# Kernel tuning notes

Measured on AMD Instinct MI355X. Metric: run time of the kernel, lower is better.

Reference implementation:

```python
import jax, jax.numpy as jnp
import numpy as np

B, K = 512, 64
EBD, VFD = 256, 512
SENS = EBD + VFD            # 768 sensory inputs to layer 0
LAYERS = [512, 256, 64]     # inter, command, motor neurons (NCP wiring)


def _make_layer_params(key, in_features, hidden):
    ks = jax.random.split(key, 9)
    cat = in_features + hidden
    s = 1.0 / np.sqrt(cat)
    def lin(k):
        return jax.random.normal(k, (hidden, cat), dtype=jnp.float32) * s
    # sparsity mask: random NCP-style sparsity on the input block, dense recurrent block
    in_mask = (jax.random.uniform(ks[8], (hidden, in_features)) < 0.5).astype(jnp.float32)
    rec_mask = jnp.ones((hidden, hidden), dtype=jnp.float32)
    mask = jnp.concatenate([in_mask, rec_mask], axis=1)  # (hidden, in+hidden)
    return dict(
        ff1_w=lin(ks[0]), ff1_b=jnp.zeros((hidden,), jnp.float32),
        ff2_w=lin(ks[1]), ff2_b=jnp.zeros((hidden,), jnp.float32),
        ta_w=lin(ks[2]), ta_b=jnp.zeros((hidden,), jnp.float32),
        tb_w=lin(ks[3]), tb_b=jnp.zeros((hidden,), jnp.float32),
        mask=mask,
    )


def setup_inputs() -> dict:
    key = jax.random.key(0)
    k_base, k_vis, k0, k1, k2 = jax.random.split(key, 5)
    inp = {
        'base_expanded_seq': jax.random.normal(k_base, (B, K, EBD), dtype=jnp.float32),
        'visual_seq': jax.random.normal(k_vis, (B, K, VFD), dtype=jnp.float32),
    }
    in_feats = [SENS, LAYERS[0], LAYERS[1]]
    for li, (k, fin, hid) in enumerate(zip([k0, k1, k2], in_feats, LAYERS)):
        p = _make_layer_params(k, fin, hid)
        for name, v in p.items():
            inp[f'l{li}_{name}'] = v
    return inp


def _cfc_cell(x_in, h, ff1_w, ff1_b, ff2_w, ff2_b, ta_w, ta_b, tb_w, tb_b, mask, ts=1.0):
    # ncps CfCCell, mode='default', no backbone, sparsity mask on ff1/ff2
    x = jnp.concatenate([x_in, h], axis=-1)          # (B, in+hidden)
    ff1 = jnp.tanh(x @ (ff1_w * mask).T + ff1_b)
    ff2 = jnp.tanh(x @ (ff2_w * mask).T + ff2_b)
    t_a = x @ ta_w.T + ta_b
    t_b = x @ tb_w.T + tb_b
    t_interp = jax.nn.sigmoid(t_a * ts + t_b)
    return ff1 * (1.0 - t_interp) + t_interp * ff2


def reference(base_expanded_seq, visual_seq,
              l0_ff1_w, l0_ff1_b, l0_ff2_w, l0_ff2_b, l0_ta_w, l0_ta_b, l0_tb_w, l0_tb_b, l0_mask,
              l1_ff1_w, l1_ff1_b, l1_ff2_w, l1_ff2_b, l1_ta_w, l1_ta_b, l1_tb_w, l1_tb_b, l1_mask,
              l2_ff1_w, l2_ff1_b, l2_ff2_w, l2_ff2_b, l2_ta_w, l2_ta_b, l2_tb_w, l2_tb_b, l2_mask):
    layers = [
        (l0_ff1_w, l0_ff1_b, l0_ff2_w, l0_ff2_b, l0_ta_w, l0_ta_b, l0_tb_w, l0_tb_b, l0_mask),
        (l1_ff1_w, l1_ff1_b, l1_ff2_w, l1_ff2_b, l1_ta_w, l1_ta_b, l1_tb_w, l1_tb_b, l1_mask),
        (l2_ff1_w, l2_ff1_b, l2_ff2_w, l2_ff2_b, l2_ta_w, l2_ta_b, l2_tb_w, l2_tb_b, l2_mask),
    ]
    b = base_expanded_seq.shape[0]
    x_seq = jnp.concatenate([base_expanded_seq, visual_seq], axis=-1)  # (B,K,768)
    x_seq = jnp.swapaxes(x_seq, 0, 1)                                  # (K,B,768)
    h_init = tuple(jnp.zeros((b, h), dtype=x_seq.dtype) for h in LAYERS)

    def step(carry, x_t):
        inp = x_t
        new_hs = []
        for p, h in zip(layers, carry):
            h_new = _cfc_cell(inp, h, *p)
            inp = h_new
            new_hs.append(h_new)
        return tuple(new_hs), None

    final_h, _ = jax.lax.scan(step, h_init, x_seq)
    return final_h[-1]  # (B, motor_neurons) = last timestep motor-layer output
```

## Files before the change

### kernel.cpp

```cpp
#include <hip/hip_runtime.h>
#include <cmath>


typedef __attribute__((ext_vector_type(8))) _Float16 half8;
typedef __attribute__((ext_vector_type(4))) float f32x4;

#define DEVINL __device__ __forceinline__

struct Params {
  const float* base;
  const float* visual;
  const _Float16 *w0, *w1, *w2;
  const float *b0f1,*b0f2,*b0ta,*b0tb;
  const float *b1f1,*b1f2,*b1ta,*b1tb;
  const float *b2f1,*b2f2,*b2ta,*b2tb;
  _Float16 *xh0,*xl0,*xh1,*xl1;
  float *xacc0,*xacc1;
  _Float16 *h0h0,*h0h1,*h0l0,*h0l1;
  _Float16 *h1h0,*h1h1,*h1l0,*h1l1;
  _Float16 *h2h0,*h2h1,*h2l0,*h2l1;
  float* out;
};

DEVINL void gload(half8& d, const _Float16* a) {
  asm volatile("global_load_dwordx4 %0, %1, off" : "=v"(d) : "v"(a));
}
template <int V>
DEVINL void vmwait() {
  __builtin_amdgcn_s_waitcnt((V & 15) | (7 << 4) | (15 << 8) | ((V >> 4) << 14));
  __builtin_amdgcn_sched_barrier(0);
}

template <int C, int NC, int D, class AF>
DEVINL void pipe_iter(half8 (&buf)[D][6], f32x4 (&acc)[4], const AF& addr) {
  constexpr int issued = (C + D < NC) ? (C + D) : NC;
  vmwait<6 * (issued - C - 1)>();
  {
    half8 b0 = buf[C % D][0], b1 = buf[C % D][1];
    half8 b2 = buf[C % D][2], b3 = buf[C % D][3];
    half8 ah = buf[C % D][4], al = buf[C % D][5];
    acc[0] = __builtin_amdgcn_mfma_f32_16x16x32_f16(ah, b0, acc[0], 0, 0, 0);
    acc[0] = __builtin_amdgcn_mfma_f32_16x16x32_f16(al, b0, acc[0], 0, 0, 0);
    acc[1] = __builtin_amdgcn_mfma_f32_16x16x32_f16(ah, b1, acc[1], 0, 0, 0);
    acc[1] = __builtin_amdgcn_mfma_f32_16x16x32_f16(al, b1, acc[1], 0, 0, 0);
    acc[2] = __builtin_amdgcn_mfma_f32_16x16x32_f16(ah, b2, acc[2], 0, 0, 0);
    acc[2] = __builtin_amdgcn_mfma_f32_16x16x32_f16(al, b2, acc[2], 0, 0, 0);
    acc[3] = __builtin_amdgcn_mfma_f32_16x16x32_f16(ah, b3, acc[3], 0, 0, 0);
    acc[3] = __builtin_amdgcn_mfma_f32_16x16x32_f16(al, b3, acc[3], 0, 0, 0);
  }
  if constexpr (C + D < NC) {
#pragma unroll
    for (int j = 0; j < 6; ++j) gload(buf[C % D][j], addr(C + D, j));
  }
  if constexpr (C + 1 < NC) pipe_iter<C + 1, NC, D>(buf, acc, addr);
}

template <int NC, class AF>
DEVINL void gemm_pipe(f32x4 (&acc)[4], const AF& addr) {
  constexpr int D = (NC < 6) ? NC : 6;
  half8 buf[D][6];
#pragma unroll
  for (int c = 0; c < D; ++c)
#pragma unroll
    for (int j = 0; j < 6; ++j) gload(buf[c][j], addr(c, j));
  pipe_iter<0, NC, D>(buf, acc, addr);
}

DEVINL void run_xprep(const Params& p, int t, int b ) {
  _Float16* xh = (t & 1) ? p.xh1 : p.xh0;
  _Float16* xl = (t & 1) ? p.xl1 : p.xl0;
  int tid = b * 256 + threadIdx.x;
#pragma unroll
  for (int i = tid; i < 49152; i += 12288) {
    int m = i / 96;
    int k = (i - m * 96) * 8;
    const float* src = (k < 256) ? (p.base + (m * 64 + t) * 256 + k)
                                 : (p.visual + (m * 64 + t) * 512 + (k - 256));
    const f32x4* q = (const f32x4*)src;
    f32x4 v0 = q[0], v1 = q[1];
    half8 hh, ll;
#pragma unroll
    for (int j = 0; j < 4; ++j) {
      _Float16 a = (_Float16)v0[j]; hh[j] = a;     ll[j]     = (_Float16)(v0[j] - (float)a);
      _Float16 c = (_Float16)v1[j]; hh[j + 4] = c; ll[j + 4] = (_Float16)(v1[j] - (float)c);
    }
    int off = (((m >> 4) * 24 + (k >> 5)) * 64 + ((k >> 3) & 3) * 16 + (m & 15)) * 8;
    *(half8*)(xh + off) = hh;
    *(half8*)(xl + off) = ll;
  }
}

DEVINL void run_xgemm(const Params& p, int t, int b ) {
  const _Float16* xh = (t & 1) ? p.xh1 : p.xh0;
  const _Float16* xl = (t & 1) ? p.xl1 : p.xl0;
  float* xacc = (t & 1) ? p.xacc1 : p.xacc0;
  const int lane = threadIdx.x & 63, wv = threadIdx.x >> 6;
  const int lr = lane & 15, lq = lane >> 4;
  const int mt = b >> 5, nt = b & 31;
  const int m_base = mt * 64 + wv * 16, n0 = nt * 16;
  const int mt16 = mt * 4 + wv;

  f32x4 acc[4];
#pragma unroll
  for (int g = 0; g < 4; ++g) acc[g] = f32x4{0.f, 0.f, 0.f, 0.f};

  const _Float16* wpk = p.w0 + (nt * 40) * 512 + lane * 8;
  const _Float16* apk = xh + (mt16 * 24) * 512 + lane * 8;
  const _Float16* lpk = xl + (mt16 * 24) * 512 + lane * 8;
  auto addr = [&](int c, int j) -> const _Float16* {
    if (j < 4) return wpk + (j * (32 * 40) + c) * 512;
    return ((j == 4) ? apk : lpk) + c * 512;
  };
  gemm_pipe<24>(acc, addr);

  const int n = n0 + lr;
  const int mrow = m_base + lq * 4;
#pragma unroll
  for (int g = 0; g < 4; ++g)
#pragma unroll
    for (int r = 0; r < 4; ++r)
      xacc[(mrow + r) * 2048 + g * 512 + n] = acc[g][r];
}

template <int L>
DEVINL void run_rec(const Params& p, int t, int b) {
  constexpr int HH = (L == 0) ? 512 : ((L == 1) ? 256 : 64);
  constexpr int NC = (L == 0) ? 16 : ((L == 1) ? 24 : 10);
  constexpr int NCH = HH / 32;

  const int lane = threadIdx.x & 63, wv = threadIdx.x >> 6;
  const int lr = lane & 15, lq = lane >> 4;
  int mt, nt;
  if constexpr (L == 0)      { mt = b >> 5; nt = b & 31; }
  else if constexpr (L == 1) { mt = b >> 4; nt = b & 15; }
  else                       { mt = b >> 2; nt = b & 3; }
  const int m_base = mt * 64 + wv * 16, n0 = nt * 16;
  const int mt16 = mt * 4 + wv;
  const int wbuf = t & 1;

  const _Float16 *hph, *hpl, *pah = nullptr, *pal = nullptr;
  _Float16 *oh, *ol;
  const float *bf1p, *bf2p, *btap, *btbp;
  const _Float16* wpk;
  if constexpr (L == 0) {
    wpk = p.w0 + (nt * 40) * 512 + lane * 8;
    hph = wbuf ? p.h0h0 : p.h0h1;  hpl = wbuf ? p.h0l0 : p.h0l1;
    oh  = wbuf ? p.h0h1 : p.h0h0;  ol  = wbuf ? p.h0l1 : p.h0l0;
    bf1p = p.b0f1; bf2p = p.b0f2; btap = p.b0ta; btbp = p.b0tb;
  } else if constexpr (L == 1) {
    wpk = p.w1 + (nt * 24) * 512 + lane * 8;
    pah = wbuf ? p.h0h1 : p.h0h0;  pal = wbuf ? p.h0l1 : p.h0l0;
    hph = wbuf ? p.h1h0 : p.h1h1;  hpl = wbuf ? p.h1l0 : p.h1l1;
    oh  = wbuf ? p.h1h1 : p.h1h0;  ol  = wbuf ? p.h1l1 : p.h1l0;
    bf1p = p.b1f1; bf2p = p.b1f2; btap = p.b1ta; btbp = p.b1tb;
  } else {
    wpk = p.w2 + (nt * 10) * 512 + lane * 8;
    pah = wbuf ? p.h1h1 : p.h1h0;  pal = wbuf ? p.h1l1 : p.h1l0;
    hph = wbuf ? p.h2h0 : p.h2h1;  hpl = wbuf ? p.h2l0 : p.h2l1;
    oh  = wbuf ? p.h2h1 : p.h2h0;  ol  = wbuf ? p.h2l1 : p.h2l0;
    bf1p = p.b2f1; bf2p = p.b2f2; btap = p.b2ta; btbp = p.b2tb;
  }

  f32x4 acc[4];
#pragma unroll
  for (int g = 0; g < 4; ++g) acc[g] = f32x4{0.f, 0.f, 0.f, 0.f};

  const int lane8 = lane * 8;
  auto addr = [&](int c, int j) -> const _Float16* {
    if constexpr (L == 0) {
      if (j < 4) return wpk + (j * (32 * 40) + 24 + c) * 512;
      return ((j == 4) ? hph : hpl) + (mt16 * 16 + c) * 512 + lane8;
    } else if constexpr (L == 1) {
      if (j < 4) return wpk + (j * (16 * 24) + c) * 512;
      if (c < 16) return ((j == 4) ? pah : pal) + (mt16 * 16 + c) * 512 + lane8;
      return ((j == 4) ? hph : hpl) + (mt16 * 8 + (c - 16)) * 512 + lane8;
    } else {
      if (j < 4) return wpk + (j * (4 * 10) + c) * 512;
      if (c < 8) return ((j == 4) ? pah : pal) + (mt16 * 8 + c) * 512 + lane8;
      return ((j == 4) ? hph : hpl) + (mt16 * 2 + (c - 8)) * 512 + lane8;
    }
  };
  gemm_pipe<NC>(acc, addr);

  const float* xacc = nullptr;
  if constexpr (L == 0) xacc = (t & 1) ? p.xacc1 : p.xacc0;

  const int n = n0 + lr;
  const float bff1 = bf1p[n], bff2 = bf2p[n], bta = btap[n], btb = btbp[n];
  const int obase = ((m_base >> 4) * NCH + (n >> 5)) * 512 + ((n >> 3) & 3) * 128 + (n & 7);
#pragma unroll
  for (int r = 0; r < 4; ++r) {
    const int row = m_base + lq * 4 + r;
    const int lrr = lq * 4 + r;
    float a0 = acc[0][r], a1 = acc[1][r], a2 = acc[2][r], a3 = acc[3][r];
    if constexpr (L == 0) {
      const float* xb = xacc + row * 2048 + n;
      a0 += xb[0]; a1 += xb[512]; a2 += xb[1024]; a3 += xb[1536];
    }
    float vf1 = a0 + bff1;
    float vf2 = a1 + bff2;
    float vt  = (a2 + bta) + (a3 + btb);
    float ff1 = tanhf(vf1);
    float ff2 = tanhf(vf2);
    float ti  = 1.0f / (1.0f + __expf(-vt));
    float hv  = ff1 + ti * (ff2 - ff1);
    _Float16 hh = (_Float16)hv;
    oh[obase + lrr * 8] = hh;
    ol[obase + lrr * 8] = (_Float16)(hv - (float)hh);
    if constexpr (L == 2) {
      if (t == 63) p.out[row * 64 + n] = hv;
    }
  }
}

__global__ __launch_bounds__(256, 2) void cfc_step(Params p, int s) {
  const int bid = blockIdx.x;
  if (bid < 48)       { int t = s + 2; if (t >= 0 && t < 64) run_xprep(p, t, bid); }
  else if (bid < 304) { int t = s + 1; if (t >= 0 && t < 64) run_xgemm(p, t, bid - 48); }
  else if (bid < 560) { int t = s;     if (t >= 0 && t < 64) run_rec<0>(p, t, bid - 304); }
  else if (bid < 688) { int t = s - 1; if (t >= 0 && t < 64) run_rec<1>(p, t, bid - 560); }
  else                { int t = s - 2; if (t >= 0 && t < 64) run_rec<2>(p, t, bid - 688); }
}

__global__ void prep_w_pk(const float* __restrict__ w, const float* __restrict__ mask,
                          _Float16* __restrict__ dst, int WK, int total) {
  int i = blockIdx.x * 256 + threadIdx.x;
  if (i >= total) return;
  int e = i & 7, lane = (i >> 3) & 63, rem = i >> 9;
  int NCk = WK >> 5;
  int c = rem % NCk, nt = rem / NCk;
  int n = nt * 16 + (lane & 15);
  int k = c * 32 + (lane >> 4) * 8 + e;
  float v = w[n * WK + k];
  if (mask) v *= mask[n * WK + k];
  dst[i] = (_Float16)v;
}

__global__ void zero_kernel(unsigned* __restrict__ p, int n) {
  int i = blockIdx.x * 256 + threadIdx.x;
  if (i < n) p[i] = 0u;
}

extern "C" void kernel_launch(void* const* d_in, const int* in_sizes, int n_in,
                              void* d_out, int out_size, void* d_ws, size_t ws_size,
                              hipStream_t stream) {
  _Float16* w0  = (_Float16*)d_ws;
  _Float16* w1  = w0 + 2621440;
  _Float16* w2  = w1 + 786432;
  _Float16* xh0 = w2 + 81920;
  _Float16* xl0 = xh0 + 393216;
  _Float16* xh1 = xl0 + 393216;
  _Float16* xl1 = xh1 + 393216;
  _Float16* hb  = xl1 + 393216;
  _Float16* h0h0 = hb;            _Float16* h0h1 = h0h0 + 262144;
  _Float16* h0l0 = h0h1 + 262144; _Float16* h0l1 = h0l0 + 262144;
  _Float16* h1h0 = h0l1 + 262144; _Float16* h1h1 = h1h0 + 131072;
  _Float16* h1l0 = h1h1 + 131072; _Float16* h1l1 = h1l0 + 131072;
  _Float16* h2h0 = h1l1 + 131072; _Float16* h2h1 = h2h0 + 32768;
  _Float16* h2l0 = h2h1 + 32768;  _Float16* h2l1 = h2l0 + 32768;
  float* xacc0 = (float*)(h2l1 + 32768);
  float* xacc1 = xacc0 + 1048576;

  const int h_uints = 1703936 / 2;
  zero_kernel<<<(h_uints + 255) / 256, 256, 0, stream>>>((unsigned*)hb, h_uints);

  const float* F = nullptr;
  auto in = [&](int i) { return (const float*)d_in[i]; };

  prep_w_pk<<<2560, 256, 0, stream>>>(in(2),  in(10), w0 + 0 * 655360, 1280, 655360);
  prep_w_pk<<<2560, 256, 0, stream>>>(in(4),  in(10), w0 + 1 * 655360, 1280, 655360);
  prep_w_pk<<<2560, 256, 0, stream>>>(in(6),  F,      w0 + 2 * 655360, 1280, 655360);
  prep_w_pk<<<2560, 256, 0, stream>>>(in(8),  F,      w0 + 3 * 655360, 1280, 655360);
  prep_w_pk<<<768,  256, 0, stream>>>(in(11), in(19), w1 + 0 * 196608, 768,  196608);
  prep_w_pk<<<768,  256, 0, stream>>>(in(13), in(19), w1 + 1 * 196608, 768,  196608);
  prep_w_pk<<<768,  256, 0, stream>>>(in(15), F,      w1 + 2 * 196608, 768,  196608);
  prep_w_pk<<<768,  256, 0, stream>>>(in(17), F,      w1 + 3 * 196608, 768,  196608);
  prep_w_pk<<<80,   256, 0, stream>>>(in(20), in(28), w2 + 0 * 20480,  320,  20480);
  prep_w_pk<<<80,   256, 0, stream>>>(in(22), in(28), w2 + 1 * 20480,  320,  20480);
  prep_w_pk<<<80,   256, 0, stream>>>(in(24), F,      w2 + 2 * 20480,  320,  20480);
  prep_w_pk<<<80,   256, 0, stream>>>(in(26), F,      w2 + 3 * 20480,  320,  20480);

  Params p;
  p.base = in(0); p.visual = in(1);
  p.w0 = w0; p.w1 = w1; p.w2 = w2;
  p.b0f1 = in(3);  p.b0f2 = in(5);  p.b0ta = in(7);  p.b0tb = in(9);
  p.b1f1 = in(12); p.b1f2 = in(14); p.b1ta = in(16); p.b1tb = in(18);
  p.b2f1 = in(21); p.b2f2 = in(23); p.b2ta = in(25); p.b2tb = in(27);
  p.xh0 = xh0; p.xl0 = xl0; p.xh1 = xh1; p.xl1 = xl1;
  p.xacc0 = xacc0; p.xacc1 = xacc1;
  p.h0h0 = h0h0; p.h0h1 = h0h1; p.h0l0 = h0l0; p.h0l1 = h0l1;
  p.h1h0 = h1h0; p.h1h1 = h1h1; p.h1l0 = h1l0; p.h1l1 = h1l1;
  p.h2h0 = h2h0; p.h2h1 = h2h1; p.h2l0 = h2l0; p.h2l1 = h2l1;
  p.out = (float*)d_out;

  for (int s = -2; s < 66; ++s) {
    cfc_step<<<720, 256, 0, stream>>>(p, s);
  }
}
```

Baseline: 1.216 ms.

## Widen per-wave GEMM tile to 64 rows to reuse weight fragments

Each wave now computes four 16-row sub-tiles against the same four weight fragments, so weight loads are reused across 64 batch rows instead of 16. The grid shrinks from 720 to 216 blocks and the load pipeline depth drops from 6 to 2 stages of 12 loads each. This cuts redundant weight traffic, but it raises register pressure (64 accumulator floats plus 24 buffered half8s) and leaves fewer blocks to hide latency across the CUs.

Result: slower. 1.361 ms (+12.0%).

```diff
diff --git a/kernel.cpp b/kernel.cpp
--- a/kernel.cpp
+++ b/kernel.cpp
@@ -32,37 +32,37 @@
 }
 
 template <int C, int NC, int D, class AF>
-DEVINL void pipe_iter(half8 (&buf)[D][6], f32x4 (&acc)[4], const AF& addr) {
+DEVINL void pipe_iter(half8 (&buf)[D][12], f32x4 (&acc)[4][4], const AF& addr) {
   constexpr int issued = (C + D < NC) ? (C + D) : NC;
-  vmwait<6 * (issued - C - 1)>();
+  vmwait<12 * (issued - C - 1)>();
   {
-    half8 b0 = buf[C % D][0], b1 = buf[C % D][1];
-    half8 b2 = buf[C % D][2], b3 = buf[C % D][3];
-    half8 ah = buf[C % D][4], al = buf[C % D][5];
-    acc[0] = __builtin_amdgcn_mfma_f32_16x16x32_f16(ah, b0, acc[0], 0, 0, 0);
-    acc[0] = __builtin_amdgcn_mfma_f32_16x16x32_f16(al, b0, acc[0], 0, 0, 0);
-    acc[1] = __builtin_amdgcn_mfma_f32_16x16x32_f16(ah, b1, acc[1], 0, 0, 0);
-    acc[1] = __builtin_amdgcn_mfma_f32_16x16x32_f16(al, b1, acc[1], 0, 0, 0);
-    acc[2] = __builtin_amdgcn_mfma_f32_16x16x32_f16(ah, b2, acc[2], 0, 0, 0);
-    acc[2] = __builtin_amdgcn_mfma_f32_16x16x32_f16(al, b2, acc[2], 0, 0, 0);
-    acc[3] = __builtin_amdgcn_mfma_f32_16x16x32_f16(ah, b3, acc[3], 0, 0, 0);
-    acc[3] = __builtin_amdgcn_mfma_f32_16x16x32_f16(al, b3, acc[3], 0, 0, 0);
+    half8 (&B)[12] = buf[C % D];
+#pragma unroll
+    for (int s = 0; s < 4; ++s)
+#pragma unroll
+      for (int g = 0; g < 4; ++g)
+        acc[s][g] = __builtin_amdgcn_mfma_f32_16x16x32_f16(B[4 + s], B[g], acc[s][g], 0, 0, 0);
+#pragma unroll
+    for (int s = 0; s < 4; ++s)
+#pragma unroll
+      for (int g = 0; g < 4; ++g)
+        acc[s][g] = __builtin_amdgcn_mfma_f32_16x16x32_f16(B[8 + s], B[g], acc[s][g], 0, 0, 0);
   }
   if constexpr (C + D < NC) {
 #pragma unroll
-    for (int j = 0; j < 6; ++j) gload(buf[C % D][j], addr(C + D, j));
+    for (int j = 0; j < 12; ++j) gload(buf[C % D][j], addr(C + D, j));
   }
   if constexpr (C + 1 < NC) pipe_iter<C + 1, NC, D>(buf, acc, addr);
 }
 
 template <int NC, class AF>
-DEVINL void gemm_pipe(f32x4 (&acc)[4], const AF& addr) {
-  constexpr int D = (NC < 6) ? NC : 6;
-  half8 buf[D][6];
+DEVINL void gemm_pipe(f32x4 (&acc)[4][4], const AF& addr) {
+  constexpr int D = (NC < 2) ? NC : 2;
+  half8 buf[D][12];
 #pragma unroll
   for (int c = 0; c < D; ++c)
 #pragma unroll
-    for (int j = 0; j < 6; ++j) gload(buf[c][j], addr(c, j));
+    for (int j = 0; j < 12; ++j) gload(buf[c][j], addr(c, j));
   pipe_iter<0, NC, D>(buf, acc, addr);
 }
 
@@ -96,30 +96,34 @@
   float* xacc = (t & 1) ? p.xacc1 : p.xacc0;
   const int lane = threadIdx.x & 63, wv = threadIdx.x >> 6;
   const int lr = lane & 15, lq = lane >> 4;
-  const int mt = b >> 5, nt = b & 31;
-  const int m_base = mt * 64 + wv * 16, n0 = nt * 16;
-  const int mt16 = mt * 4 + wv;
-
-  f32x4 acc[4];
-#pragma unroll
-  for (int g = 0; g < 4; ++g) acc[g] = f32x4{0.f, 0.f, 0.f, 0.f};
+  const int mt = b >> 3, nt = (b & 7) * 4 + wv;
+
+  f32x4 acc[4][4];
+#pragma unroll
+  for (int s = 0; s < 4; ++s)
+#pragma unroll
+    for (int g = 0; g < 4; ++g) acc[s][g] = f32x4{0.f, 0.f, 0.f, 0.f};
 
   const _Float16* wpk = p.w0 + (nt * 40) * 512 + lane * 8;
-  const _Float16* apk = xh + (mt16 * 24) * 512 + lane * 8;
-  const _Float16* lpk = xl + (mt16 * 24) * 512 + lane * 8;
+  const _Float16* ah0 = xh + ((mt * 4) * 24) * 512 + lane * 8;
+  const _Float16* al0 = xl + ((mt * 4) * 24) * 512 + lane * 8;
   auto addr = [&](int c, int j) -> const _Float16* {
     if (j < 4) return wpk + (j * (32 * 40) + c) * 512;
-    return ((j == 4) ? apk : lpk) + c * 512;
+    if (j < 8) return ah0 + ((j - 4) * 24 + c) * 512;
+    return al0 + ((j - 8) * 24 + c) * 512;
   };
   gemm_pipe<24>(acc, addr);
 
-  const int n = n0 + lr;
-  const int mrow = m_base + lq * 4;
-#pragma unroll
-  for (int g = 0; g < 4; ++g)
-#pragma unroll
-    for (int r = 0; r < 4; ++r)
-      xacc[(mrow + r) * 2048 + g * 512 + n] = acc[g][r];
+  const int n = nt * 16 + lr;
+#pragma unroll
+  for (int s = 0; s < 4; ++s) {
+    const int mrow = mt * 64 + s * 16 + lq * 4;
+#pragma unroll
+    for (int g = 0; g < 4; ++g)
+#pragma unroll
+      for (int r = 0; r < 4; ++r)
+        xacc[(mrow + r) * 2048 + g * 512 + n] = acc[s][g][r];
+  }
 }
 
 template <int L>
@@ -131,11 +135,9 @@
   const int lane = threadIdx.x & 63, wv = threadIdx.x >> 6;
   const int lr = lane & 15, lq = lane >> 4;
   int mt, nt;
-  if constexpr (L == 0)      { mt = b >> 5; nt = b & 31; }
-  else if constexpr (L == 1) { mt = b >> 4; nt = b & 15; }
-  else                       { mt = b >> 2; nt = b & 3; }
-  const int m_base = mt * 64 + wv * 16, n0 = nt * 16;
-  const int mt16 = mt * 4 + wv;
+  if constexpr (L == 0)      { mt = b >> 3; nt = (b & 7) * 4 + wv; }
+  else if constexpr (L == 1) { mt = b >> 2; nt = (b & 3) * 4 + wv; }
+  else                       { mt = b;      nt = wv; }
   const int wbuf = t & 1;
 
   const _Float16 *hph, *hpl, *pah = nullptr, *pal = nullptr;
@@ -161,23 +163,31 @@
     bf1p = p.b2f1; bf2p = p.b2f2; btap = p.b2ta; btbp = p.b2tb;
   }
 
-  f32x4 acc[4];
-#pragma unroll
-  for (int g = 0; g < 4; ++g) acc[g] = f32x4{0.f, 0.f, 0.f, 0.f};
+  f32x4 acc[4][4];
+#pragma unroll
+  for (int s = 0; s < 4; ++s)
+#pragma unroll
+    for (int g = 0; g < 4; ++g) acc[s][g] = f32x4{0.f, 0.f, 0.f, 0.f};
 
   const int lane8 = lane * 8;
+  const int mt4 = mt * 4;
   auto addr = [&](int c, int j) -> const _Float16* {
     if constexpr (L == 0) {
       if (j < 4) return wpk + (j * (32 * 40) + 24 + c) * 512;
-      return ((j == 4) ? hph : hpl) + (mt16 * 16 + c) * 512 + lane8;
+      if (j < 8) return hph + ((mt4 + (j - 4)) * 16 + c) * 512 + lane8;
+      return hpl + ((mt4 + (j - 8)) * 16 + c) * 512 + lane8;
     } else if constexpr (L == 1) {
       if (j < 4) return wpk + (j * (16 * 24) + c) * 512;
-      if (c < 16) return ((j == 4) ? pah : pal) + (mt16 * 16 + c) * 512 + lane8;
-      return ((j == 4) ? hph : hpl) + (mt16 * 8 + (c - 16)) * 512 + lane8;
+      const int s = (j < 8) ? (j - 4) : (j - 8);
+      const bool hi = (j < 8);
+      if (c < 16) return (hi ? pah : pal) + ((mt4 + s) * 16 + c) * 512 + lane8;
+      return (hi ? hph : hpl) + ((mt4 + s) * 8 + (c - 16)) * 512 + lane8;
     } else {
       if (j < 4) return wpk + (j * (4 * 10) + c) * 512;
-      if (c < 8) return ((j == 4) ? pah : pal) + (mt16 * 8 + c) * 512 + lane8;
-      return ((j == 4) ? hph : hpl) + (mt16 * 2 + (c - 8)) * 512 + lane8;
+      const int s = (j < 8) ? (j - 4) : (j - 8);
+      const bool hi = (j < 8);
+      if (c < 8) return (hi ? pah : pal) + ((mt4 + s) * 8 + c) * 512 + lane8;
+      return (hi ? hph : hpl) + ((mt4 + s) * 2 + (c - 8)) * 512 + lane8;
     }
   };
   gemm_pipe<NC>(acc, addr);
@@ -185,30 +195,34 @@
   const float* xacc = nullptr;
   if constexpr (L == 0) xacc = (t & 1) ? p.xacc1 : p.xacc0;
 
-  const int n = n0 + lr;
+  const int n = nt * 16 + lr;
   const float bff1 = bf1p[n], bff2 = bf2p[n], bta = btap[n], btb = btbp[n];
-  const int obase = ((m_base >> 4) * NCH + (n >> 5)) * 512 + ((n >> 3) & 3) * 128 + (n & 7);
-#pragma unroll
-  for (int r = 0; r < 4; ++r) {
-    const int row = m_base + lq * 4 + r;
-    const int lrr = lq * 4 + r;
-    float a0 = acc[0][r], a1 = acc[1][r], a2 = acc[2][r], a3 = acc[3][r];
-    if constexpr (L == 0) {
-      const float* xb = xacc + row * 2048 + n;
-      a0 += xb[0]; a1 += xb[512]; a2 += xb[1024]; a3 += xb[1536];
-    }
-    float vf1 = a0 + bff1;
-    float vf2 = a1 + bff2;
-    float vt  = (a2 + bta) + (a3 + btb);
-    float ff1 = tanhf(vf1);
-    float ff2 = tanhf(vf2);
-    float ti  = 1.0f / (1.0f + __expf(-vt));
-    float hv  = ff1 + ti * (ff2 - ff1);
-    _Float16 hh = (_Float16)hv;
-    oh[obase + lrr * 8] = hh;
-    ol[obase + lrr * 8] = (_Float16)(hv - (float)hh);
-    if constexpr (L == 2) {
-      if (t == 63) p.out[row * 64 + n] = hv;
+#pragma unroll
+  for (int s = 0; s < 4; ++s) {
+    const int mt16s = mt4 + s;
+    const int obase = (mt16s * NCH + (n >> 5)) * 512 + ((n >> 3) & 3) * 128 + (n & 7);
+#pragma unroll
+    for (int r = 0; r < 4; ++r) {
+      const int row = mt * 64 + s * 16 + lq * 4 + r;
+      const int lrr = lq * 4 + r;
+      float a0 = acc[s][0][r], a1 = acc[s][1][r], a2 = acc[s][2][r], a3 = acc[s][3][r];
+      if constexpr (L == 0) {
+        const float* xb = xacc + row * 2048 + n;
+        a0 += xb[0]; a1 += xb[512]; a2 += xb[1024]; a3 += xb[1536];
+      }
+      float vf1 = a0 + bff1;
+      float vf2 = a1 + bff2;
+      float vt  = (a2 + bta) + (a3 + btb);
+      float ff1 = tanhf(vf1);
+      float ff2 = tanhf(vf2);
+      float ti  = 1.0f / (1.0f + __expf(-vt));
+      float hv  = ff1 + ti * (ff2 - ff1);
+      _Float16 hh = (_Float16)hv;
+      oh[obase + lrr * 8] = hh;
+      ol[obase + lrr * 8] = (_Float16)(hv - (float)hh);
+      if constexpr (L == 2) {
+        if (t == 63) p.out[row * 64 + n] = hv;
+      }
     }
   }
 }
@@ -216,10 +230,10 @@
 __global__ __launch_bounds__(256, 2) void cfc_step(Params p, int s) {
   const int bid = blockIdx.x;
   if (bid < 48)       { int t = s + 2; if (t >= 0 && t < 64) run_xprep(p, t, bid); }
-  else if (bid < 304) { int t = s + 1; if (t >= 0 && t < 64) run_xgemm(p, t, bid - 48); }
-  else if (bid < 560) { int t = s;     if (t >= 0 && t < 64) run_rec<0>(p, t, bid - 304); }
-  else if (bid < 688) { int t = s - 1; if (t >= 0 && t < 64) run_rec<1>(p, t, bid - 560); }
-  else                { int t = s - 2; if (t >= 0 && t < 64) run_rec<2>(p, t, bid - 688); }
+  else if (bid < 112) { int t = s + 1; if (t >= 0 && t < 64) run_xgemm(p, t, bid - 48); }
+  else if (bid < 176) { int t = s;     if (t >= 0 && t < 64) run_rec<0>(p, t, bid - 112); }
+  else if (bid < 208) { int t = s - 1; if (t >= 0 && t < 64) run_rec<1>(p, t, bid - 176); }
+  else                { int t = s - 2; if (t >= 0 && t < 64) run_rec<2>(p, t, bid - 208); }
 }
 
 __global__ void prep_w_pk(const float* __restrict__ w, const float* __restrict__ mask,
@@ -294,6 +308,6 @@
   p.out = (float*)d_out;
 
   for (int s = -2; s < 66; ++s) {
-    cfc_step<<<720, 256, 0, stream>>>(p, s);
-  }
-}
+    cfc_step<<<216, 256, 0, stream>>>(p, s);
+  }
+}
```
